# Performance work log

Measured on AMD Instinct MI355X. Metric: run time of the kernel, lower is better.

The kernel has to match this reference:

```python
import jax, jax.numpy as jnp
import numpy as np
from jax import lax

N_FFT = 1024
HOP = 256
FFT_BIN = N_FFT // 2 + 1  # 513


def make_stft_kernel(n_fft: int) -> jnp.ndarray:
    """Fixed DFT basis kernel, shape (2*fft_bin, 1, n_fft), windowed with periodic Hann."""
    fft_bin = n_fft // 2 + 1
    # torch.linspace(0, 1, n_fft) is endpoint-inclusive, same as jnp.linspace
    t = jnp.linspace(0.0, 1.0, n_fft, dtype=jnp.float32)[None, None, :]
    k = jnp.arange(fft_bin, dtype=jnp.float32)[:, None, None]
    xt = t * k * (2.0 * jnp.pi)
    kernel = jnp.concatenate([jnp.cos(xt), jnp.sin(xt)], axis=0)  # (2*fft_bin, 1, n_fft)
    # torch.hann_window is periodic: 0.5*(1 - cos(2*pi*n/N))
    n = jnp.arange(n_fft, dtype=jnp.float32)
    hann = 0.5 * (1.0 - jnp.cos(2.0 * jnp.pi * n / n_fft))
    return kernel * hann[None, None, :]


def setup_inputs() -> dict:
    key = jax.random.key(0)
    x = jax.random.normal(key, (16, 1, 262144), dtype=jnp.float32)
    kernel = make_stft_kernel(N_FFT)
    return {"x": x, "kernel": kernel}


def reference(x, kernel):
    # padding == 'center'
    left = N_FFT // 2
    right = N_FFT - left
    x = jnp.pad(x, ((0, 0), (0, 0), (left, right)))
    # strided conv1d with fixed DFT-basis kernel
    y = lax.conv_general_dilated(
        x, kernel,
        window_strides=(HOP,),
        padding='VALID',
        dimension_numbers=('NCW', 'OIW', 'NCW'),
    )  # (B, 2*fft_bin, num_frames)
    real, imag = jnp.split(y, 2, axis=1)
    return real, imag
```

## Files before the change

kernel.cpp:

```cpp
#include <hip/hip_runtime.h>
#include <hip/hip_bf16.h>

#define NFFT    1024
#define HOPSZ   256
#define XLEN    262144
#define PADLEN  (XLEN + NFFT)
#define NBATCH  16
#define NBINS2  1026
#define FBIN    513
#define NFRAMES 1025
#define NGF     (NBATCH * NFRAMES)
#define TOTOUT  ((size_t)NBATCH * FBIN * NFRAMES)

#define KT 64
#define NKT 16
#define NT_TILES 64
#define MT_TILES 4
#define NWG (MT_TILES * NT_TILES)
#define ABYTES 32768
#define BUFE   32768
#define BUFB   65536
#define NTAIL  49184
#define PSTRIDE 130
#define LDS_BYTES (256 * PSTRIDE * 4)

typedef short bf16x8 __attribute__((ext_vector_type(8)));
typedef float f32x4  __attribute__((ext_vector_type(4)));
typedef unsigned short u16x8 __attribute__((ext_vector_type(8)));
typedef unsigned short u16x4 __attribute__((ext_vector_type(4)));

__device__ __forceinline__ unsigned short f2bf(float f) {
  union { float f; unsigned u; } v; v.f = f;
  unsigned r = v.u + 0x7fffu + ((v.u >> 16) & 1u);
  return (unsigned short)(r >> 16);
}
__device__ __forceinline__ float bf2f(unsigned short h) {
  union { unsigned u; float f; } v; v.u = ((unsigned)h) << 16; return v.f;
}

typedef __attribute__((address_space(1))) void void_g;
typedef __attribute__((address_space(3))) void void_l;
__device__ __forceinline__ void gload_lds16(const void* g, void* l) {
  __builtin_amdgcn_global_load_lds((void_g*)(g), (void_l*)(l), 16, 0, 0);
}

__global__ __launch_bounds__(256) void pack_x_kernel(const float* __restrict__ x,
                                                     unsigned short* __restrict__ xp) {
  long long t = (long long)blockIdx.x * 256 + threadIdx.x;
  long long base = t * 8;
  if (base >= (long long)NBATCH * PADLEN) return;
  int b   = (int)(base / PADLEN);
  int pos = (int)(base % PADLEN);
  const float* xb = x + (long long)b * XLEN;
  u16x8 v;
#pragma unroll
  for (int j = 0; j < 8; ++j) {
    int xi = pos + j - (NFFT / 2);
    float f = ((unsigned)xi < (unsigned)XLEN) ? xb[xi] : 0.0f;
    v[j] = f2bf(f);
  }
  *reinterpret_cast<u16x8*>(xp + base) = v;
}

__global__ __launch_bounds__(256) void pack_w_kernel(const float* __restrict__ W,
                                                     unsigned short* __restrict__ Wb) {
  long long t = ((long long)blockIdx.x * 256 + threadIdx.x) * 4;
  if (t >= (long long)NBINS2 * NFFT) return;
  float4 f = *reinterpret_cast<const float4*>(W + t);
  u16x4 v;
  v[0] = f2bf(f.x); v[1] = f2bf(f.y); v[2] = f2bf(f.z); v[3] = f2bf(f.w);
  *reinterpret_cast<u16x4*>(Wb + t) = v;
}

__global__ __launch_bounds__(512, 2) void stft_mfma8_kernel(const unsigned short* __restrict__ Xp,
                                                            const unsigned short* __restrict__ Wb,
                                                            float* __restrict__ out) {
  extern __shared__ unsigned short lds[];
  const int tid = threadIdx.x;
  const int l   = tid & 63;
  const int w   = tid >> 6;
  const int wr  = w >> 2;
  const int wc  = w & 3;
  const int r16 = l & 15, hi = l >> 4;

  const int bid = blockIdx.x;
  const int c_  = bid >> 3;
  const int nt  = (bid & 7) * 8 + (c_ & 7);
  const int mt  = c_ >> 3;
  const int bin0 = mt * 256;
  const int gf0  = nt * 256;

  const int lr = l >> 3;
  const int ls = l & 7;
  const int cswz = ((ls ^ lr) << 3);

  unsigned aqoff[4];
#pragma unroll
  for (int qi = 0; qi < 4; ++qi)
    aqoff[qi] = (unsigned)(bin0 + qi * 64 + w * 8 + lr) * NFFT + cswz;
  unsigned boff[4];
#pragma unroll
  for (int j = 0; j < 4; ++j) {
    const int gf = gf0 + (w * 4 + j) * 8 + lr;
    const int bb = gf / NFRAMES;
    const int fr = gf - bb * NFRAMES;
    boff[j] = (unsigned)bb * PADLEN + (unsigned)fr * HOPSZ + cswz;
  }

#define STG_Q(D, QI, KC) gload_lds16(Wb + aqoff[QI] + (KC), lds + (D) * BUFE + (QI) * 4096 + w * 512)
#define STG_B(D, KC) do { \
    _Pragma("unroll") \
    for (int j_ = 0; j_ < 4; ++j_) \
      gload_lds16(Xp + boff[j_] + (KC), lds + (D) * BUFE + 16384 + (w * 4 + j_) * 512); \
    } while (0)

  const int aB0 = (wr * 128 + r16) * 128;
  const int bB0 = ABYTES + (wc * 64 + r16) * 128;
  const int swz = (r16 & 7) << 4;
  const int c0  = (hi * 16) ^ swz;
  const int c1  = (64 + hi * 16) ^ swz;

#define RD_A(BASE, MH, C) do { \
    _Pragma("unroll") \
    for (int m_ = 0; m_ < 4; ++m_) \
      Aq[m_] = *reinterpret_cast<const bf16x8*>((BASE) + aB0 + (MH) * 8192 + m_ * 2048 + (C)); \
    } while (0)
#define RD_B(BASE, C) do { \
    _Pragma("unroll") \
    for (int n_ = 0; n_ < 4; ++n_) \
      Bq[n_] = *reinterpret_cast<const bf16x8*>((BASE) + bB0 + n_ * 2048 + (C)); \
    } while (0)

#define MFMA16(MLO) do { \
    __builtin_amdgcn_s_setprio(1); \
    _Pragma("unroll") \
    for (int m_ = 0; m_ < 4; ++m_) { \
      _Pragma("unroll") \
      for (int n_ = 0; n_ < 4; ++n_) \
        acc[(MLO) + m_][n_] = __builtin_amdgcn_mfma_f32_16x16x32_bf16(Aq[m_], Bq[n_], acc[(MLO) + m_][n_], 0, 0, 0); \
    } \
    __builtin_amdgcn_s_setprio(0); } while (0)

  f32x4 acc[8][4] = {};
  bf16x8 Aq[4], Bq[4];

  STG_Q(0, 0, 0); STG_Q(0, 1, 0); STG_Q(0, 2, 0); STG_Q(0, 3, 0); STG_B(0, 0);
  STG_Q(1, 0, KT); STG_Q(1, 2, KT); STG_B(1, KT);
  asm volatile("s_waitcnt vmcnt(6)" ::: "memory");
  __builtin_amdgcn_s_barrier();
  __builtin_amdgcn_sched_barrier(0);

  for (int t = 0; t < NKT; ++t) {
    const int c = t & 1, n = c ^ 1;
    const char* base = (const char*)lds + c * BUFB;
    const int kc1 = (t + 1) << 6;
    const int kc2 = (t + 2) << 6;

    if (t < NKT - 1) asm volatile("s_waitcnt vmcnt(6)" ::: "memory");
    else             asm volatile("s_waitcnt vmcnt(0)" ::: "memory");
    __builtin_amdgcn_sched_barrier(0);
    RD_A(base, 0, c0);
    RD_B(base, c0);
    __builtin_amdgcn_s_barrier();
    if (t < NKT - 1) { STG_Q(n, 1, kc1); STG_Q(n, 3, kc1); }
    asm volatile("s_waitcnt lgkmcnt(0)" ::: "memory");
    __builtin_amdgcn_sched_barrier(0);
    MFMA16(0);

    RD_A(base, 1, c0);
    __builtin_amdgcn_s_barrier();
    asm volatile("s_waitcnt lgkmcnt(0)" ::: "memory");
    __builtin_amdgcn_sched_barrier(0);
    MFMA16(4);

    RD_A(base, 0, c1);
    RD_B(base, c1);
    __builtin_amdgcn_s_barrier();
    asm volatile("s_waitcnt lgkmcnt(0)" ::: "memory");
    __builtin_amdgcn_sched_barrier(0);
    MFMA16(0);

    RD_A(base, 1, c1);
    __builtin_amdgcn_s_barrier();
    if (t < NKT - 2) { STG_Q(c, 0, kc2); STG_Q(c, 2, kc2); STG_B(c, kc2); }
    asm volatile("s_waitcnt lgkmcnt(0)" ::: "memory");
    __builtin_amdgcn_sched_barrier(0);
    MFMA16(4);
  }

  {
    float* patch = (float*)lds;
    const int col     = l & 15;
    const int rbase   = (l >> 4) * 4;
    const int h_mine  = wc >> 1;
    const int colbase = (wc & 1) * 64;

#pragma unroll
    for (int h = 0; h < 2; ++h) {
      __builtin_amdgcn_s_barrier();
      if (h_mine == h) {
#pragma unroll
        for (int m = 0; m < 8; ++m)
#pragma unroll
          for (int n2 = 0; n2 < 4; ++n2)
#pragma unroll
            for (int r = 0; r < 4; ++r)
              patch[(wr * 128 + m * 16 + rbase + r) * PSTRIDE + colbase + n2 * 16 + col] =
                  acc[m][n2][r];
      }
      __builtin_amdgcn_s_barrier();

      size_t baseR[2];
      int cols[2];
#pragma unroll
      for (int j = 0; j < 2; ++j) {
        const int gf = gf0 + h * 128 + j * 64 + l;
        const int bb = gf / NFRAMES;
        const int fr = gf - bb * NFRAMES;
        baseR[j] = (size_t)bb * FBIN * NFRAMES + fr;
        cols[j]  = h * 128 + j * 64 + l;
      }
      for (int i = 0; i < 32; ++i) {
        const int row = i * 8 + w;
        const int bin = bin0 + row;
        const size_t binoff = (size_t)bin * NFRAMES;
#pragma unroll
        for (int j = 0; j < 2; ++j) {
          const float v = patch[row * PSTRIDE + cols[j] - h * 128];
          size_t off = binoff + (bin < FBIN ? baseR[j]
                                            : baseR[j] + TOTOUT - (size_t)FBIN * NFRAMES);
          out[off] = v;
        }
      }
    }
  }
#undef STG_Q
#undef STG_B
#undef RD_A
#undef RD_B
#undef MFMA16
}

__global__ __launch_bounds__(512) void stft_tail_kernel(const unsigned short* __restrict__ Xp,
                                                        const unsigned short* __restrict__ Wb,
                                                        float* __restrict__ out) {
  const int wid = (int)((blockIdx.x * 512 + threadIdx.x) >> 6);
  const int l   = threadIdx.x & 63;
  if (wid >= NTAIL) return;
  int bin, gf;
  if (wid < 2 * NGF) { bin = 1024 + (wid & 1); gf = wid >> 1; }
  else { const int s = wid - 2 * NGF; gf = 16384 + (s & 15); bin = s >> 4; }
  const int bb = gf / NFRAMES;
  const int fr = gf - bb * NFRAMES;
  const unsigned short* xr = Xp + (size_t)bb * PADLEN + (size_t)fr * HOPSZ + l * 16;
  const unsigned short* wr = Wb + (size_t)bin * NFFT + l * 16;
  u16x8 x0 = *reinterpret_cast<const u16x8*>(xr);
  u16x8 x1 = *reinterpret_cast<const u16x8*>(xr + 8);
  u16x8 w0 = *reinterpret_cast<const u16x8*>(wr);
  u16x8 w1 = *reinterpret_cast<const u16x8*>(wr + 8);
  float s0 = 0.f, s1 = 0.f;
#pragma unroll
  for (int j = 0; j < 8; ++j) {
    s0 = fmaf(bf2f(x0[j]), bf2f(w0[j]), s0);
    s1 = fmaf(bf2f(x1[j]), bf2f(w1[j]), s1);
  }
  float s = s0 + s1;
#pragma unroll
  for (int k = 32; k >= 1; k >>= 1) s += __shfl_xor(s, k);
  if (l == 0) {
    size_t off;
    if (bin < FBIN) off = ((size_t)bb * FBIN + bin) * NFRAMES + fr;
    else            off = TOTOUT + ((size_t)bb * FBIN + (bin - FBIN)) * NFRAMES + fr;
    out[off] = s;
  }
}

__global__ void stft_direct_kernel(const float* __restrict__ x, const float* __restrict__ W,
                                   float* __restrict__ out,
                                   int bin_lo, int nbins, int fr_lo, int nframes) {
  long long total = (long long)NBATCH * nbins * nframes;
  for (long long t = (long long)blockIdx.x * blockDim.x + threadIdx.x; t < total;
       t += (long long)gridDim.x * blockDim.x) {
    int fr = fr_lo + (int)(t % nframes);
    long long q = t / nframes;
    int bin = bin_lo + (int)(q % nbins);
    int b   = (int)(q / nbins);
    const float* xb = x + (long long)b * XLEN;
    const float* wrow = W + (long long)bin * NFFT;
    float s = 0.f;
    const int base = fr * HOPSZ - (NFFT / 2);
    for (int j = 0; j < NFFT; ++j) {
      int xi = base + j;
      float xv = ((unsigned)xi < (unsigned)XLEN) ? xb[xi] : 0.f;
      s = fmaf(xv, wrow[j], s);
    }
    size_t off;
    if (bin < FBIN) off = ((size_t)b * FBIN + bin) * NFRAMES + fr;
    else            off = TOTOUT + ((size_t)b * FBIN + (bin - FBIN)) * NFRAMES + fr;
    out[off] = s;
  }
}

extern "C" void kernel_launch(void* const* d_in, const int* in_sizes, int n_in,
                              void* d_out, int out_size, void* d_ws, size_t ws_size,
                              hipStream_t stream) {
  const float* x = (const float*)d_in[0];
  const float* W = (const float*)d_in[1];
  float* out = (float*)d_out;

  const size_t xp_bytes = (size_t)NBATCH * PADLEN * sizeof(unsigned short);
  const size_t wb_bytes = (size_t)NBINS2 * NFFT * sizeof(unsigned short);

  if (ws_size >= xp_bytes + wb_bytes) {
    unsigned short* xp = (unsigned short*)d_ws;
    unsigned short* wb = (unsigned short*)((char*)d_ws + xp_bytes);

    {
      long long threads = (long long)NBATCH * PADLEN / 8;
      pack_x_kernel<<<(int)((threads + 255) / 256), 256, 0, stream>>>(x, xp);
    }
    pack_w_kernel<<<(NBINS2 * NFFT / 4 + 255) / 256, 256, 0, stream>>>(W, wb);

    stft_mfma8_kernel<<<NWG, 512, LDS_BYTES, stream>>>(xp, wb, out);
    stft_tail_kernel<<<NTAIL / 8, 512, 0, stream>>>(xp, wb, out);
  } else {
    stft_direct_kernel<<<2048, 256, 0, stream>>>(x, W, out, 0, NBINS2, 0, NFRAMES);
  }
}
```

Baseline: 69.18 us.

## Restructure GEMM main loop into register double-buffered LDS reads with one barrier

Replaces the four-phase main loop, which had a barrier and an LDS wait before each of four 16-MFMA groups, with a two-phase schedule. Full A/B fragments for the next k-half are read into a second register set while 32 MFMAs run on the current set, leaving one barrier per k-tile. Global-to-LDS staging now issues whole tiles at once. This doubles fragment register usage and waits for all global loads each iteration, which may raise register pressure or reduce latency hiding. The epilogue patch stride changes from 130 to 132 floats, along with a simplified column index.

```diff
diff --git a/kernel.cpp b/kernel.cpp
--- a/kernel.cpp
+++ b/kernel.cpp
@@ -21,7 +21,7 @@
 #define BUFE   32768
 #define BUFB   65536
 #define NTAIL  49184
-#define PSTRIDE 130
+#define PSTRIDE 132
 #define LDS_BYTES (256 * PSTRIDE * 4)
 
 typedef short bf16x8 __attribute__((ext_vector_type(8)));
@@ -107,8 +107,10 @@
     boff[j] = (unsigned)bb * PADLEN + (unsigned)fr * HOPSZ + cswz;
   }
 
-#define STG_Q(D, QI, KC) gload_lds16(Wb + aqoff[QI] + (KC), lds + (D) * BUFE + (QI) * 4096 + w * 512)
-#define STG_B(D, KC) do { \
+#define STAGE(D, KC) do { \
+    _Pragma("unroll") \
+    for (int q_ = 0; q_ < 4; ++q_) \
+      gload_lds16(Wb + aqoff[q_] + (KC), lds + (D) * BUFE + q_ * 4096 + w * 512); \
     _Pragma("unroll") \
     for (int j_ = 0; j_ < 4; ++j_) \
       gload_lds16(Xp + boff[j_] + (KC), lds + (D) * BUFE + 16384 + (w * 4 + j_) * 512); \
@@ -120,72 +122,55 @@
   const int c0  = (hi * 16) ^ swz;
   const int c1  = (64 + hi * 16) ^ swz;
 
-#define RD_A(BASE, MH, C) do { \
-    _Pragma("unroll") \
-    for (int m_ = 0; m_ < 4; ++m_) \
-      Aq[m_] = *reinterpret_cast<const bf16x8*>((BASE) + aB0 + (MH) * 8192 + m_ * 2048 + (C)); \
+#define RD12(BASE, C, AARR, BARR) do { \
+    _Pragma("unroll") \
+    for (int n_ = 0; n_ < 4; ++n_) \
+      BARR[n_] = *reinterpret_cast<const bf16x8*>((const char*)(BASE) + bB0 + n_ * 2048 + (C)); \
+    _Pragma("unroll") \
+    for (int m_ = 0; m_ < 8; ++m_) \
+      AARR[m_] = *reinterpret_cast<const bf16x8*>((const char*)(BASE) + aB0 + m_ * 2048 + (C)); \
     } while (0)
-#define RD_B(BASE, C) do { \
-    _Pragma("unroll") \
-    for (int n_ = 0; n_ < 4; ++n_) \
-      Bq[n_] = *reinterpret_cast<const bf16x8*>((BASE) + bB0 + n_ * 2048 + (C)); \
-    } while (0)
-
-#define MFMA16(MLO) do { \
+
+#define MFMA32(AARR, BARR) do { \
     __builtin_amdgcn_s_setprio(1); \
     _Pragma("unroll") \
-    for (int m_ = 0; m_ < 4; ++m_) { \
+    for (int m_ = 0; m_ < 8; ++m_) { \
       _Pragma("unroll") \
       for (int n_ = 0; n_ < 4; ++n_) \
-        acc[(MLO) + m_][n_] = __builtin_amdgcn_mfma_f32_16x16x32_bf16(Aq[m_], Bq[n_], acc[(MLO) + m_][n_], 0, 0, 0); \
+        acc[m_][n_] = __builtin_amdgcn_mfma_f32_16x16x32_bf16(AARR[m_], BARR[n_], acc[m_][n_], 0, 0, 0); \
     } \
     __builtin_amdgcn_s_setprio(0); } while (0)
 
   f32x4 acc[8][4] = {};
-  bf16x8 Aq[4], Bq[4];
-
-  STG_Q(0, 0, 0); STG_Q(0, 1, 0); STG_Q(0, 2, 0); STG_Q(0, 3, 0); STG_B(0, 0);
-  STG_Q(1, 0, KT); STG_Q(1, 2, KT); STG_B(1, KT);
-  asm volatile("s_waitcnt vmcnt(6)" ::: "memory");
+  bf16x8 A0[8], B0[4], A1[8], B1[4];
+
+  STAGE(0, 0);
+  STAGE(1, KT);
+  asm volatile("s_waitcnt vmcnt(8)" ::: "memory");
   __builtin_amdgcn_s_barrier();
   __builtin_amdgcn_sched_barrier(0);
+  RD12(lds, c0, A0, B0);
 
   for (int t = 0; t < NKT; ++t) {
-    const int c = t & 1, n = c ^ 1;
-    const char* base = (const char*)lds + c * BUFB;
-    const int kc1 = (t + 1) << 6;
+    const int ci = t & 1;
+    const char* cbuf = (const char*)lds + ci * BUFB;
+    const char* nbuf = (const char*)lds + (ci ^ 1) * BUFB;
     const int kc2 = (t + 2) << 6;
 
-    if (t < NKT - 1) asm volatile("s_waitcnt vmcnt(6)" ::: "memory");
-    else             asm volatile("s_waitcnt vmcnt(0)" ::: "memory");
-    __builtin_amdgcn_sched_barrier(0);
-    RD_A(base, 0, c0);
-    RD_B(base, c0);
+    RD12(cbuf, c1, A1, B1);
+    __builtin_amdgcn_sched_barrier(0);
+    asm volatile("s_waitcnt lgkmcnt(12)" ::: "memory");
+    __builtin_amdgcn_sched_barrier(0);
+    MFMA32(A0, B0);
+
+    asm volatile("s_waitcnt vmcnt(0) lgkmcnt(0)" ::: "memory");
+    __builtin_amdgcn_sched_barrier(0);
     __builtin_amdgcn_s_barrier();
-    if (t < NKT - 1) { STG_Q(n, 1, kc1); STG_Q(n, 3, kc1); }
-    asm volatile("s_waitcnt lgkmcnt(0)" ::: "memory");
-    __builtin_amdgcn_sched_barrier(0);
-    MFMA16(0);
-
-    RD_A(base, 1, c0);
-    __builtin_amdgcn_s_barrier();
-    asm volatile("s_waitcnt lgkmcnt(0)" ::: "memory");
-    __builtin_amdgcn_sched_barrier(0);
-    MFMA16(4);
-
-    RD_A(base, 0, c1);
-    RD_B(base, c1);
-    __builtin_amdgcn_s_barrier();
-    asm volatile("s_waitcnt lgkmcnt(0)" ::: "memory");
-    __builtin_amdgcn_sched_barrier(0);
-    MFMA16(0);
-
-    RD_A(base, 1, c1);
-    __builtin_amdgcn_s_barrier();
-    if (t < NKT - 2) { STG_Q(c, 0, kc2); STG_Q(c, 2, kc2); STG_B(c, kc2); }
-    asm volatile("s_waitcnt lgkmcnt(0)" ::: "memory");
-    __builtin_amdgcn_sched_barrier(0);
-    MFMA16(4);
+    __builtin_amdgcn_sched_barrier(0);
+    if (t < NKT - 1) RD12(nbuf, c0, A0, B0);
+    if (t < NKT - 2) STAGE(ci, kc2);
+    __builtin_amdgcn_sched_barrier(0);
+    MFMA32(A1, B1);
   }
 
   {
@@ -218,7 +203,7 @@
         const int bb = gf / NFRAMES;
         const int fr = gf - bb * NFRAMES;
         baseR[j] = (size_t)bb * FBIN * NFRAMES + fr;
-        cols[j]  = h * 128 + j * 64 + l;
+        cols[j]  = j * 64 + l;
       }
       for (int i = 0; i < 32; ++i) {
         const int row = i * 8 + w;
@@ -226,7 +211,7 @@
         const size_t binoff = (size_t)bin * NFRAMES;
 #pragma unroll
         for (int j = 0; j < 2; ++j) {
-          const float v = patch[row * PSTRIDE + cols[j] - h * 128];
+          const float v = patch[row * PSTRIDE + cols[j]];
           size_t off = binoff + (bin < FBIN ? baseR[j]
                                             : baseR[j] + TOTOUT - (size_t)FBIN * NFRAMES);
           out[off] = v;
@@ -234,11 +219,9 @@
       }
     }
   }
-#undef STG_Q
-#undef STG_B
-#undef RD_A
-#undef RD_B
-#undef MFMA16
+#undef STAGE
+#undef RD12
+#undef MFMA32
 }
 
 __global__ __launch_bounds__(512) void stft_tail_kernel(const unsigned short* __restrict__ Xp,
```

Result: no change. 69.39 us (+0.3%).
